# Optimization experiments

Measured on AMD Instinct MI355X. Metric: run time of the kernel, lower is better.

## Reference

```python
import jax, jax.numpy as jnp
import numpy as np
import math

B, S, D = 2, 2048, 512
N_BUCKETS = 64
N_HYP = int(math.log2(N_BUCKETS))  # 6


def setup_inputs() -> dict:
    key = jax.random.key(0)
    ks = jax.random.split(key, 6)
    x = jax.random.normal(ks[0], (B, S, D), dtype=jnp.float32)
    # torch.nn.Linear params: weight [out,in], bias [out]
    Wq = jax.random.normal(ks[1], (D, D), dtype=jnp.float32) / jnp.sqrt(D)
    bq = jax.random.normal(ks[2], (D,), dtype=jnp.float32) * 0.01
    Wv = jax.random.normal(ks[3], (D, D), dtype=jnp.float32) / jnp.sqrt(D)
    bv = jax.random.normal(ks[4], (D,), dtype=jnp.float32) * 0.01
    hyperplanes = jax.random.normal(ks[5], (D + 1, N_HYP), dtype=jnp.float32)
    return {"x": x, "Wq": Wq, "bq": bq, "Wv": Wv, "bv": bv, "hyperplanes": hyperplanes}


def _get_buckets(q, hyperplanes):
    # append constant-1 feature: [B,S,D+1]
    qa = jnp.concatenate([q, jnp.ones(q.shape[:2] + (1,), q.dtype)], axis=2)
    proj = jnp.einsum('bse,en->bsn', qa, hyperplanes)
    bits = (proj >= 0).astype(jnp.float32)
    powers = (2.0 ** jnp.arange(N_HYP)).astype(jnp.float32)
    return jnp.einsum('bsn,n->bs', bits, powers)  # [B,S] float bucket ids


def reference(x, Wq, bq, Wv, bv, hyperplanes):
    q = x @ Wq.T + bq
    v = x @ Wv.T + bv
    buckets = _get_buckets(q, hyperplanes)  # [B,S]
    scale = 1.0 / math.sqrt(D)

    def body(acc, i):
        # NOTE: faithful to source: tokens IN bucket i are zeroed (masked_fill
        # with mask = buckets == i), then full dense softmax attention.
        mask = (buckets == i)[..., None]  # [B,S,1]
        qb = jnp.where(mask, 0.0, q)
        vb = jnp.where(mask, 0.0, v)
        att = jax.nn.softmax(jnp.einsum('bsd,btd->bst', qb, qb) * scale, axis=-1)
        return acc + jnp.einsum('bst,btd->bsd', att, vb), None

    init = jnp.zeros_like(x)
    out, _ = jax.lax.scan(body, init, jnp.arange(N_BUCKETS, dtype=jnp.float32))
    return out
```

## Files before the change

kernel.cpp:

```cpp
#include <hip/hip_runtime.h>
#include <math.h>

#define B_ 2
#define S_ 2048
#define D_ 512
#define NB_ 64
#define NH_ 6
#define ROWS (B_*S_)
#define SCALE 0.044194173824159216f

typedef float f32x4 __attribute__((ext_vector_type(4)));
typedef __bf16 bf16v8 __attribute__((ext_vector_type(8)));
typedef short s16x8 __attribute__((ext_vector_type(8)));
typedef unsigned short u16x4 __attribute__((ext_vector_type(4)));

__device__ __forceinline__ float b2f(unsigned short u) {
    unsigned int v = (unsigned int)u << 16;
    float f; __builtin_memcpy(&f, &v, 4); return f;
}
__device__ __forceinline__ unsigned short f2b(float f) {
    unsigned int v; __builtin_memcpy(&v, &f, 4);
    v += 0x7fffu + ((v >> 16) & 1u);
    return (unsigned short)(v >> 16);
}

#define GLOAD16(g, l) __builtin_amdgcn_global_load_lds( \
    (const __attribute__((address_space(1))) unsigned int*)(g), \
    (__attribute__((address_space(3))) unsigned int*)(uintptr_t)(l), 16, 0, 0)

template<int EPI>
__global__ __launch_bounds__(256) void mfma_nt(
    const unsigned short* __restrict__ A, const unsigned short* __restrict__ B,
    int N, int K, long long zA, long long zB,
    float* __restrict__ Cf, long long zC,
    unsigned short* __restrict__ Ch, long long zCh,
    const float* __restrict__ e0, long long z0,
    const float* __restrict__ e1, long long z1,
    const int* __restrict__ ib, long long zi,
    const int* __restrict__ prm)
{
    __shared__ unsigned short Als[128 * 64];
    __shared__ unsigned short Bls[64 * 64];
    int tid = threadIdx.x;
    int w = tid >> 6, l = tid & 63;
    int wr = w >> 1, wc = w & 1;
    int zb = blockIdx.z;
    A += zb * zA;  B += zb * zB;
    if (prm) prm += (size_t)zb * S_;

    int gx = gridDim.x;
    int nwg = gx * gridDim.y;
    int lin = blockIdx.y * gx + blockIdx.x;
    int qq = nwg >> 3;
    int wg = (lin & 7) * qq + (lin >> 3);
    int m0 = (wg / gx) * 128, n0 = (wg % gx) * 64;

    const unsigned short* asrc[4];
    #pragma unroll
    for (int j = 0; j < 4; ++j) {
        int chunk = w * 4 + j;
        int r = chunk * 8 + (l >> 3);
        asrc[j] = A + (size_t)(m0 + r) * K + ((l & 7) ^ (l >> 3)) * 8;
    }
    const unsigned short* bsrc[2];
    #pragma unroll
    for (int j = 0; j < 2; ++j) {
        int chunk = w * 2 + j;
        int r = n0 + chunk * 8 + (l >> 3);
        if (prm) r = prm[r];
        bsrc[j] = B + (size_t)r * K + ((l & 7) ^ (l >> 3)) * 8;
    }

    f32x4 acc[4][2] = {};
    int rl = l & 15, hi = l >> 4;

    for (int k0 = 0; k0 < K; k0 += 64) {
        #pragma unroll
        for (int j = 0; j < 4; ++j) GLOAD16(asrc[j] + k0, Als + (w * 4 + j) * 512);
        #pragma unroll
        for (int j = 0; j < 2; ++j) GLOAD16(bsrc[j] + k0, Bls + (w * 2 + j) * 512);
        __syncthreads();
        bf16v8 af[4][2], bfr[2][2];
        const char* Ab = (const char*)Als;
        const char* Bb = (const char*)Bls;
        #pragma unroll
        for (int kk = 0; kk < 2; ++kk) {
            int kb = kk * 64 + hi * 16;
            #pragma unroll
            for (int f = 0; f < 4; ++f) {
                int ra = wr * 64 + f * 16 + rl;
                af[f][kk] = *(const bf16v8*)(Ab + ra * 128 + (kb ^ ((ra & 7) << 4)));
            }
            #pragma unroll
            for (int f = 0; f < 2; ++f) {
                int rb = wc * 32 + f * 16 + rl;
                bfr[f][kk] = *(const bf16v8*)(Bb + rb * 128 + (kb ^ ((rb & 7) << 4)));
            }
        }
        #pragma unroll
        for (int fm = 0; fm < 4; ++fm)
            #pragma unroll
            for (int fn = 0; fn < 2; ++fn)
                #pragma unroll
                for (int kk = 0; kk < 2; ++kk)
                    acc[fm][fn] = __builtin_amdgcn_mfma_f32_16x16x32_bf16(
                        af[fm][kk], bfr[fn][kk], acc[fm][fn], 0, 0, 0);
        __syncthreads();
    }

    if (EPI == 0) {
        int colBase = n0 + wc * 32;
        if (colBase < D_) {
            #pragma unroll
            for (int fm = 0; fm < 4; ++fm) {
                float p[4] = {0.f, 0.f, 0.f, 0.f};
                #pragma unroll
                for (int fn = 0; fn < 2; ++fn) {
                    int col = colBase + fn * 16 + rl;
                    float bs = e0[col];
                    #pragma unroll
                    for (int r = 0; r < 4; ++r) {
                        int row = m0 + wr * 64 + fm * 16 + hi * 4 + r;
                        float cv = acc[fm][fn][r] + bs;
                        unsigned short h = f2b(cv);
                        Ch[(size_t)row * D_ + col] = h;
                        float qb = b2f(h);
                        p[r] = fmaf(qb, qb, p[r]);
                    }
                }
                #pragma unroll
                for (int mask = 1; mask < 16; mask <<= 1)
                    #pragma unroll
                    for (int r = 0; r < 4; ++r) p[r] += __shfl_xor(p[r], mask);
                if (rl == 0) {
                    #pragma unroll
                    for (int r = 0; r < 4; ++r) {
                        int row = m0 + wr * 64 + fm * 16 + hi * 4 + r;
                        atomicAdd(&Cf[row], p[r]);
                    }
                }
            }
        } else {
            #pragma unroll
            for (int fm = 0; fm < 4; ++fm)
                #pragma unroll
                for (int fn = 0; fn < 2; ++fn) {
                    int col = colBase + fn * 16 + rl - D_;
                    float bs = e1[col];
                    #pragma unroll
                    for (int r = 0; r < 4; ++r) {
                        int row = m0 + wr * 64 + fm * 16 + hi * 4 + r;
                        ((float*)ib)[(size_t)row * D_ + col] = acc[fm][fn][r] + bs;
                    }
                }
        }
    } else {
        Ch += zb * zCh;  e0 += zb * z0;
        #pragma unroll
        for (int fm = 0; fm < 4; ++fm)
            #pragma unroll
            for (int fn = 0; fn < 2; ++fn) {
                int col = n0 + wc * 32 + fn * 16 + rl;
                #pragma unroll
                for (int r = 0; r < 4; ++r) {
                    int row = m0 + wr * 64 + fm * 16 + hi * 4 + r;
                    float ev = __expf(fmaf(acc[fm][fn][r], SCALE, -e0[row]));
                    Ch[(size_t)row * N + col] = f2b(ev);
                }
            }
    }
}

__global__ __launch_bounds__(256) void mfma_pv64(
    const unsigned short* __restrict__ Eh, const unsigned short* __restrict__ vT,
    const float* __restrict__ sumVall, const float* __restrict__ sumVb,
    const int* __restrict__ bucket, float* __restrict__ out)
{
    __shared__ unsigned short Als[64 * 64];
    __shared__ unsigned short Bls[64 * 64];
    int tid = threadIdx.x, w = tid >> 6, l = tid & 63;
    int wr = w >> 1, wc = w & 1, rl = l & 15, hi = l >> 4;
    int zb = blockIdx.z;
    const unsigned short* A  = Eh + (size_t)zb * S_ * S_;
    const unsigned short* Bv = vT + (size_t)zb * D_ * S_;
    const float* sva = sumVall + (size_t)zb * D_;
    const float* svb = sumVb + (size_t)zb * NB_ * D_;
    const int* bkt = bucket + (size_t)zb * S_;
    float* outb = out + (size_t)zb * S_ * D_;

    int lin = blockIdx.y * 8 + blockIdx.x;
    int xcd = lin & 7, rest = lin >> 3;
    int m0 = (((rest >> 3) << 3) | xcd) * 64;
    int n0 = (rest & 7) * 64;

    const unsigned short* asrc[2];
    const unsigned short* bsrc[2];
    #pragma unroll
    for (int j = 0; j < 2; ++j) {
        int chunk = w * 2 + j;
        int r = chunk * 8 + (l >> 3);
        int c = ((l & 7) ^ (l >> 3)) * 8;
        asrc[j] = A  + (size_t)(m0 + r) * S_ + c;
        bsrc[j] = Bv + (size_t)(n0 + r) * S_ + c;
    }

    f32x4 acc[2][2] = {};
    for (int k0 = 0; k0 < S_; k0 += 64) {
        #pragma unroll
        for (int j = 0; j < 2; ++j) GLOAD16(asrc[j] + k0, Als + (w * 2 + j) * 512);
        #pragma unroll
        for (int j = 0; j < 2; ++j) GLOAD16(bsrc[j] + k0, Bls + (w * 2 + j) * 512);
        __syncthreads();
        bf16v8 af[2][2], bfr[2][2];
        const char* Ab = (const char*)Als;
        const char* Bb = (const char*)Bls;
        #pragma unroll
        for (int kk = 0; kk < 2; ++kk) {
            int kb = kk * 64 + hi * 16;
            #pragma unroll
            for (int f = 0; f < 2; ++f) {
                int ra = wr * 32 + f * 16 + rl;
                af[f][kk] = *(const bf16v8*)(Ab + ra * 128 + (kb ^ ((ra & 7) << 4)));
                int rb = wc * 32 + f * 16 + rl;
                bfr[f][kk] = *(const bf16v8*)(Bb + rb * 128 + (kb ^ ((rb & 7) << 4)));
            }
        }
        #pragma unroll
        for (int fm = 0; fm < 2; ++fm)
            #pragma unroll
            for (int fn = 0; fn < 2; ++fn)
                #pragma unroll
                for (int kk = 0; kk < 2; ++kk)
                    acc[fm][fn] = __builtin_amdgcn_mfma_f32_16x16x32_bf16(
                        af[fm][kk], bfr[fn][kk], acc[fm][fn], 0, 0, 0);
        __syncthreads();
    }
    const float invS = 1.0f / (float)S_;
    #pragma unroll
    for (int fm = 0; fm < 2; ++fm)
        #pragma unroll
        for (int fn = 0; fn < 2; ++fn) {
            int col = n0 + wc * 32 + fn * 16 + rl;
            float sa = sva[col];
            #pragma unroll
            for (int r = 0; r < 4; ++r) {
                int row = m0 + wr * 32 + fm * 16 + hi * 4 + r;
                int bm = bkt[row];
                outb[(size_t)row * D_ + col] =
                    acc[fm][fn][r] + (sa - svb[(size_t)bm * D_ + col]) * invS;
            }
        }
}

__global__ void init_kernel(float* __restrict__ Mrow, int* __restrict__ cnt)
{
    int i = blockIdx.x * 256 + threadIdx.x;
    if (i < ROWS) Mrow[i] = 0.f;
    if (i < B_ * NB_) cnt[i] = 0;
}

__global__ void convert_bf16(const float* __restrict__ src, unsigned short* __restrict__ dst, int n)
{
    for (int i = (blockIdx.x * 256 + threadIdx.x) * 4; i < n; i += gridDim.x * 1024) {
        float4 f = *(const float4*)(src + i);
        u16x4 u = { f2b(f.x), f2b(f.y), f2b(f.z), f2b(f.w) };
        *(u16x4*)(dst + i) = u;
    }
}

__global__ __launch_bounds__(256) void transpose_v(
    const float* __restrict__ v, const int* __restrict__ perm,
    unsigned short* __restrict__ vT)
{
    __shared__ float tl[32][33];
    int b = blockIdx.z;
    int d0 = blockIdx.x * 32, s0 = blockIdx.y * 32;
    int tx = threadIdx.x & 31, ty = threadIdx.x >> 5;
    const float* vb = v + (size_t)b * S_ * D_;
    const int* pm = perm + (size_t)b * S_;
    #pragma unroll
    for (int i = 0; i < 4; ++i)
        tl[ty + i * 8][tx] = vb[(size_t)pm[s0 + ty + i * 8] * D_ + d0 + tx];
    __syncthreads();
    unsigned short* vt = vT + (size_t)b * D_ * S_;
    #pragma unroll
    for (int i = 0; i < 4; ++i)
        vt[(size_t)(d0 + ty + i * 8) * S_ + s0 + tx] = f2b(tl[tx][ty + i * 8]);
}

__global__ __launch_bounds__(64) void bucket_kernel(
    const unsigned short* __restrict__ qh, const float* __restrict__ H,
    int* __restrict__ bucket, float* __restrict__ Mrow)
{
    int row = blockIdx.x;
    int lane = threadIdx.x;
    const unsigned short* qr = qh + (size_t)row * D_;
    float proj[NH_] = {};
    for (int d = lane; d < D_; d += 64) {
        float qv = b2f(qr[d]);
        #pragma unroll
        for (int n = 0; n < NH_; ++n)
            proj[n] = fmaf(qv, H[d * NH_ + n], proj[n]);
    }
    #pragma unroll
    for (int off = 32; off; off >>= 1) {
        #pragma unroll
        for (int n = 0; n < NH_; ++n) proj[n] += __shfl_down(proj[n], off);
    }
    if (lane == 0) {
        int bk = 0;
        #pragma unroll
        for (int n = 0; n < NH_; ++n) {
            float p = proj[n] + H[D_ * NH_ + n];
            if (p >= 0.f) bk |= (1 << n);
        }
        bucket[row] = bk;
        Mrow[row] = Mrow[row] * SCALE;
    }
}

__global__ __launch_bounds__(256) void hist_kernel(
    const int* __restrict__ bucket, int* __restrict__ cnt, int* __restrict__ idxl)
{
    int r = blockIdx.x * 256 + threadIdx.x;
    int b = r / S_;
    int s = r - b * S_;
    int j = bucket[r];
    int pos = atomicAdd(&cnt[b * NB_ + j], 1);
    idxl[((size_t)(b * NB_ + j)) * S_ + pos] = s;
}

__global__ __launch_bounds__(64) void prefix_kernel(
    const int* __restrict__ cnt, int* __restrict__ off)
{
    int b = blockIdx.x;
    int j = threadIdx.x;
    int c = cnt[b * NB_ + j];
    int x = c;
    #pragma unroll
    for (int o = 1; o < 64; o <<= 1) {
        int y = __shfl_up(x, o);
        if (j >= o) x += y;
    }
    off[b * (NB_ + 1) + j] = x - c;
    if (j == 63) off[b * (NB_ + 1) + 64] = x;
}

__global__ __launch_bounds__(64) void permbuild_kernel(
    const int* __restrict__ idxl, const int* __restrict__ cnt,
    const int* __restrict__ off, int* __restrict__ perm, int* __restrict__ p2b)
{
    int j = blockIdx.x, b = blockIdx.y;
    int n = cnt[b * NB_ + j];
    int o = off[b * (NB_ + 1) + j];
    const int* lst = idxl + ((size_t)(b * NB_ + j)) * S_;
    for (int k = threadIdx.x; k < n; k += 64) {
        perm[(size_t)b * S_ + o + k] = lst[k];
        p2b[(size_t)b * S_ + o + k] = j;
    }
}

__global__ __launch_bounds__(256) void zwgamma_kernel(
    unsigned short* __restrict__ Eh, const int* __restrict__ p2b,
    const int* __restrict__ off, const int* __restrict__ cnt,
    const int* __restrict__ bucket, const float* __restrict__ Mrow)
{
    int row = blockIdx.x;
    int b = row >> 11;
    __shared__ float er[S_];
    __shared__ float zl[NB_];
    __shared__ float wl[NB_ + 1];
    int tid = threadIdx.x;
    unsigned short* Er = Eh + (size_t)row * S_;
    int t0 = tid * 8;
    s16x8 ev = *(const s16x8*)(Er + t0);
    #pragma unroll
    for (int i = 0; i < 8; ++i)
        er[t0 + i] = b2f((unsigned short)ev[i]);
    __syncthreads();
    {
        int j = tid >> 2, sub = tid & 3;
        int lo = off[b * (NB_ + 1) + j], hiX = off[b * (NB_ + 1) + j + 1];
        float z = 0.f;
        for (int k = lo + sub; k < hiX; k += 4) z += er[k];
        z += __shfl_xor(z, 1);
        z += __shfl_xor(z, 2);
        if (sub == 0) zl[j] = z;
    }
    __syncthreads();
    if (tid < NB_) {
        int j = tid;
        float zj = zl[j];
        float ztot = zj;
        #pragma unroll
        for (int o = 32; o; o >>= 1) ztot += __shfl_xor(ztot, o);
        int bs = bucket[row];
        float em = __expf(-Mrow[row]);
        float wj = 0.f;
        if (j != bs) wj = 1.0f / (ztot - zj + (float)cnt[b * NB_ + j] * em);
        float Wt = wj;
        #pragma unroll
        for (int o = 32; o; o >>= 1) Wt += __shfl_xor(Wt, o);
        wl[j] = wj;
        if (j == 0) wl[NB_] = Wt;
    }
    __syncthreads();
    float Wt = wl[NB_];
    const int* pb = p2b + (size_t)b * S_ + t0;
    int4 b0 = *(const int4*)pb;
    int4 b1 = *(const int4*)(pb + 4);
    s16x8 ov;
    ov[0] = (short)f2b(er[t0 + 0] * (Wt - wl[b0.x]));
    ov[1] = (short)f2b(er[t0 + 1] * (Wt - wl[b0.y]));
    ov[2] = (short)f2b(er[t0 + 2] * (Wt - wl[b0.z]));
    ov[3] = (short)f2b(er[t0 + 3] * (Wt - wl[b0.w]));
    ov[4] = (short)f2b(er[t0 + 4] * (Wt - wl[b1.x]));
    ov[5] = (short)f2b(er[t0 + 5] * (Wt - wl[b1.y]));
    ov[6] = (short)f2b(er[t0 + 6] * (Wt - wl[b1.z]));
    ov[7] = (short)f2b(er[t0 + 7] * (Wt - wl[b1.w]));
    *(s16x8*)(Er + t0) = ov;
}

__global__ __launch_bounds__(256) void sumv2_kernel(
    const float* __restrict__ v, const int* __restrict__ cnt,
    const int* __restrict__ idxl, float* __restrict__ sumVb)
{
    int j = blockIdx.x, b = blockIdx.y;
    int d = blockIdx.z * 256 + threadIdx.x;
    int n = cnt[b * NB_ + j];
    const int* lst = idxl + ((size_t)(b * NB_ + j)) * S_;
    const float* vb = v + (size_t)b * S_ * D_;
    float acc = 0.f;
    for (int k = 0; k < n; ++k)
        acc += vb[(size_t)lst[k] * D_ + d];
    sumVb[((size_t)b * NB_ + j) * D_ + d] = acc;
}

__global__ __launch_bounds__(256) void sumvall_kernel(
    const float* __restrict__ sumVb, float* __restrict__ sumVall)
{
    int b = blockIdx.y;
    int d = blockIdx.x * 256 + threadIdx.x;
    float acc = 0.f;
    for (int j = 0; j < NB_; ++j)
        acc += sumVb[((size_t)b * NB_ + j) * D_ + d];
    sumVall[b * D_ + d] = acc;
}

extern "C" void kernel_launch(void* const* d_in, const int* in_sizes, int n_in,
                              void* d_out, int out_size, void* d_ws, size_t ws_size,
                              hipStream_t stream) {
    (void)in_sizes; (void)n_in; (void)out_size; (void)ws_size;
    const float* x  = (const float*)d_in[0];
    const float* Wq = (const float*)d_in[1];
    const float* bq = (const float*)d_in[2];
    const float* Wv = (const float*)d_in[3];
    const float* bv = (const float*)d_in[4];
    const float* H  = (const float*)d_in[5];
    float* out = (float*)d_out;

    char* p = (char*)d_ws;
    auto alloc = [&](size_t bytes) -> char* {
        char* r = p; p += (bytes + 255) & ~(size_t)255; return r;
    };
    float* v       = (float*)alloc((size_t)ROWS * D_ * 4);
    float* Mrow    = (float*)alloc((size_t)ROWS * 4);
    float* sumVb   = (float*)alloc((size_t)B_ * NB_ * D_ * 4);
    float* sumVall = (float*)alloc((size_t)B_ * D_ * 4);
    int*   bucket  = (int*)alloc((size_t)ROWS * 4);
    int*   cnt     = (int*)alloc((size_t)B_ * NB_ * 4);
    int*   offb    = (int*)alloc((size_t)B_ * (NB_ + 1) * 4);
    int*   perm    = (int*)alloc((size_t)B_ * S_ * 4);
    int*   p2b     = (int*)alloc((size_t)B_ * S_ * 4);
    int*   idxl    = (int*)alloc((size_t)B_ * NB_ * S_ * 4);
    unsigned short* xh   = (unsigned short*)alloc((size_t)ROWS * D_ * 2);
    unsigned short* qh   = (unsigned short*)alloc((size_t)ROWS * D_ * 2);
    unsigned short* Wqvh = (unsigned short*)alloc((size_t)2 * D_ * D_ * 2);
    unsigned short* vTh  = (unsigned short*)alloc((size_t)B_ * D_ * S_ * 2);
    unsigned short* Eh   = (unsigned short*)alloc((size_t)B_ * S_ * S_ * 2);

    init_kernel<<<ROWS / 256, 256, 0, stream>>>(Mrow, cnt);
    convert_bf16<<<2048, 256, 0, stream>>>(x, xh, ROWS * D_);
    convert_bf16<<<256, 256, 0, stream>>>(Wq, Wqvh, D_ * D_);
    convert_bf16<<<256, 256, 0, stream>>>(Wv, Wqvh + (size_t)D_ * D_, D_ * D_);
    mfma_nt<0><<<dim3(2 * D_ / 64, ROWS / 128, 1), 256, 0, stream>>>(
        xh, Wqvh, 2 * D_, D_, 0, 0, Mrow, 0, qh, 0, bq, 0, bv, 0, (int*)v, 0, nullptr);
    bucket_kernel<<<ROWS, 64, 0, stream>>>(qh, H, bucket, Mrow);
    hist_kernel<<<ROWS / 256, 256, 0, stream>>>(bucket, cnt, idxl);
    prefix_kernel<<<B_, 64, 0, stream>>>(cnt, offb);
    permbuild_kernel<<<dim3(NB_, B_), 64, 0, stream>>>(idxl, cnt, offb, perm, p2b);
    sumv2_kernel<<<dim3(NB_, B_, D_ / 256), 256, 0, stream>>>(v, cnt, idxl, sumVb);
    sumvall_kernel<<<dim3(D_ / 256, B_), 256, 0, stream>>>(sumVb, sumVall);
    transpose_v<<<dim3(D_ / 32, S_ / 32, B_), 256, 0, stream>>>(v, perm, vTh);
    mfma_nt<1><<<dim3(S_ / 64, S_ / 128, B_), 256, 0, stream>>>(
        qh, qh, S_, D_, (long long)S_ * D_, (long long)S_ * D_,
        nullptr, 0, Eh, (long long)S_ * S_, Mrow, S_, nullptr, 0, nullptr, 0, perm);
    zwgamma_kernel<<<ROWS, 256, 0, stream>>>(Eh, p2b, offb, cnt, bucket, Mrow);
    mfma_pv64<<<dim3(D_ / 64, S_ / 64, B_), 256, 0, stream>>>(
        Eh, vTh, sumVall, sumVb, bucket, out);
}
```

Measured before the change: 116.2 us.

## Merge small prep kernels and widen QK^T tile to 128x128

Folds init and the three bf16 conversions into one prep kernel. Merges the histogram into the bucket kernel and prefix with perm build, and replaces the sumVall reduction with atomics inside sumv2. Splits the templated GEMM into a projection kernel and a dedicated QK kernel whose tile grows from 128x64 to 128x128 for more reuse. This cuts launch count and global traffic, at the cost of a serial per-bucket perm loop, more registers, and fewer workgroups for the QK GEMM.

```diff
diff --git a/kernel.cpp b/kernel.cpp
--- a/kernel.cpp
+++ b/kernel.cpp
@@ -28,25 +28,44 @@
     (const __attribute__((address_space(1))) unsigned int*)(g), \
     (__attribute__((address_space(3))) unsigned int*)(uintptr_t)(l), 16, 0, 0)
 
-template<int EPI>
-__global__ __launch_bounds__(256) void mfma_nt(
+__global__ void prep_kernel(
+    const float* __restrict__ x, unsigned short* __restrict__ xh,
+    const float* __restrict__ Wq, const float* __restrict__ Wv,
+    unsigned short* __restrict__ Wqvh,
+    float* __restrict__ Mrow, int* __restrict__ cnt, float* __restrict__ sumVall)
+{
+    int t = blockIdx.x * 256 + threadIdx.x;
+    int stride = gridDim.x * 256;
+    for (int i = t; i < ROWS * D_ / 4; i += stride) {
+        float4 f = ((const float4*)x)[i];
+        u16x4 u = { f2b(f.x), f2b(f.y), f2b(f.z), f2b(f.w) };
+        ((u16x4*)xh)[i] = u;
+    }
+    for (int i = t; i < D_ * D_ / 4; i += stride) {
+        float4 f = ((const float4*)Wq)[i];
+        u16x4 u = { f2b(f.x), f2b(f.y), f2b(f.z), f2b(f.w) };
+        ((u16x4*)Wqvh)[i] = u;
+        float4 g = ((const float4*)Wv)[i];
+        u16x4 w = { f2b(g.x), f2b(g.y), f2b(g.z), f2b(g.w) };
+        ((u16x4*)(Wqvh + (size_t)D_ * D_))[i] = w;
+    }
+    for (int i = t; i < ROWS; i += stride) Mrow[i] = 0.f;
+    for (int i = t; i < B_ * NB_; i += stride) cnt[i] = 0;
+    for (int i = t; i < B_ * D_; i += stride) sumVall[i] = 0.f;
+}
+
+__global__ __launch_bounds__(256) void mfma_proj(
     const unsigned short* __restrict__ A, const unsigned short* __restrict__ B,
-    int N, int K, long long zA, long long zB,
-    float* __restrict__ Cf, long long zC,
-    unsigned short* __restrict__ Ch, long long zCh,
-    const float* __restrict__ e0, long long z0,
-    const float* __restrict__ e1, long long z1,
-    const int* __restrict__ ib, long long zi,
-    const int* __restrict__ prm)
+    const float* __restrict__ bq, const float* __restrict__ bv,
+    float* __restrict__ MrowRaw, unsigned short* __restrict__ qh,
+    float* __restrict__ v)
 {
     __shared__ unsigned short Als[128 * 64];
     __shared__ unsigned short Bls[64 * 64];
+    const int K = D_, N = 2 * D_;
     int tid = threadIdx.x;
     int w = tid >> 6, l = tid & 63;
     int wr = w >> 1, wc = w & 1;
-    int zb = blockIdx.z;
-    A += zb * zA;  B += zb * zB;
-    if (prm) prm += (size_t)zb * S_;
 
     int gx = gridDim.x;
     int nwg = gx * gridDim.y;
@@ -67,7 +86,6 @@
     for (int j = 0; j < 2; ++j) {
         int chunk = w * 2 + j;
         int r = n0 + chunk * 8 + (l >> 3);
-        if (prm) r = prm[r];
         bsrc[j] = B + (size_t)r * K + ((l & 7) ^ (l >> 3)) * 8;
     }
 
@@ -108,66 +126,134 @@
         __syncthreads();
     }
 
-    if (EPI == 0) {
-        int colBase = n0 + wc * 32;
-        if (colBase < D_) {
-            #pragma unroll
-            for (int fm = 0; fm < 4; ++fm) {
-                float p[4] = {0.f, 0.f, 0.f, 0.f};
-                #pragma unroll
-                for (int fn = 0; fn < 2; ++fn) {
-                    int col = colBase + fn * 16 + rl;
-                    float bs = e0[col];
-                    #pragma unroll
-                    for (int r = 0; r < 4; ++r) {
-                        int row = m0 + wr * 64 + fm * 16 + hi * 4 + r;
-                        float cv = acc[fm][fn][r] + bs;
-                        unsigned short h = f2b(cv);
-                        Ch[(size_t)row * D_ + col] = h;
-                        float qb = b2f(h);
-                        p[r] = fmaf(qb, qb, p[r]);
-                    }
-                }
-                #pragma unroll
-                for (int mask = 1; mask < 16; mask <<= 1)
-                    #pragma unroll
-                    for (int r = 0; r < 4; ++r) p[r] += __shfl_xor(p[r], mask);
-                if (rl == 0) {
-                    #pragma unroll
-                    for (int r = 0; r < 4; ++r) {
-                        int row = m0 + wr * 64 + fm * 16 + hi * 4 + r;
-                        atomicAdd(&Cf[row], p[r]);
-                    }
-                }
-            }
-        } else {
-            #pragma unroll
-            for (int fm = 0; fm < 4; ++fm)
-                #pragma unroll
-                for (int fn = 0; fn < 2; ++fn) {
-                    int col = colBase + fn * 16 + rl - D_;
-                    float bs = e1[col];
-                    #pragma unroll
-                    for (int r = 0; r < 4; ++r) {
-                        int row = m0 + wr * 64 + fm * 16 + hi * 4 + r;
-                        ((float*)ib)[(size_t)row * D_ + col] = acc[fm][fn][r] + bs;
-                    }
-                }
-        }
-    } else {
-        Ch += zb * zCh;  e0 += zb * z0;
-        #pragma unroll
-        for (int fm = 0; fm < 4; ++fm)
+    int colBase = n0 + wc * 32;
+    if (colBase < D_) {
+        #pragma unroll
+        for (int fm = 0; fm < 4; ++fm) {
+            float p[4] = {0.f, 0.f, 0.f, 0.f};
             #pragma unroll
             for (int fn = 0; fn < 2; ++fn) {
-                int col = n0 + wc * 32 + fn * 16 + rl;
+                int col = colBase + fn * 16 + rl;
+                float bs = bq[col];
                 #pragma unroll
                 for (int r = 0; r < 4; ++r) {
                     int row = m0 + wr * 64 + fm * 16 + hi * 4 + r;
-                    float ev = __expf(fmaf(acc[fm][fn][r], SCALE, -e0[row]));
-                    Ch[(size_t)row * N + col] = f2b(ev);
+                    float cv = acc[fm][fn][r] + bs;
+                    unsigned short h = f2b(cv);
+                    qh[(size_t)row * D_ + col] = h;
+                    float qb = b2f(h);
+                    p[r] = fmaf(qb, qb, p[r]);
                 }
             }
+            #pragma unroll
+            for (int mask = 1; mask < 16; mask <<= 1)
+                #pragma unroll
+                for (int r = 0; r < 4; ++r) p[r] += __shfl_xor(p[r], mask);
+            if (rl == 0) {
+                #pragma unroll
+                for (int r = 0; r < 4; ++r) {
+                    int row = m0 + wr * 64 + fm * 16 + hi * 4 + r;
+                    atomicAdd(&MrowRaw[row], p[r]);
+                }
+            }
+        }
+    } else {
+        #pragma unroll
+        for (int fm = 0; fm < 4; ++fm)
+            #pragma unroll
+            for (int fn = 0; fn < 2; ++fn) {
+                int col = colBase + fn * 16 + rl - D_;
+                float bs = bv[col];
+                #pragma unroll
+                for (int r = 0; r < 4; ++r) {
+                    int row = m0 + wr * 64 + fm * 16 + hi * 4 + r;
+                    v[(size_t)row * D_ + col] = acc[fm][fn][r] + bs;
+                }
+            }
+    }
+}
+
+__global__ __launch_bounds__(256) void mfma_qk(
+    const unsigned short* __restrict__ qh, const int* __restrict__ prm,
+    const float* __restrict__ Mrow, unsigned short* __restrict__ Eh)
+{
+    __shared__ unsigned short Als[128 * 64];
+    __shared__ unsigned short Bls[128 * 64];
+    const int K = D_;
+    int tid = threadIdx.x;
+    int w = tid >> 6, l = tid & 63;
+    int wr = w >> 1, wc = w & 1;
+    int zb = blockIdx.z;
+    const unsigned short* A = qh + (size_t)zb * S_ * D_;
+    prm += (size_t)zb * S_;
+    const float* Mb = Mrow + (size_t)zb * S_;
+    unsigned short* Eb = Eh + (size_t)zb * S_ * S_;
+
+    int gx = gridDim.x;
+    int nwg = gx * gridDim.y;
+    int lin = blockIdx.y * gx + blockIdx.x;
+    int qq = nwg >> 3;
+    int wg = (lin & 7) * qq + (lin >> 3);
+    int m0 = (wg / gx) * 128, n0 = (wg % gx) * 128;
+
+    const unsigned short* asrc[4];
+    const unsigned short* bsrc[4];
+    #pragma unroll
+    for (int j = 0; j < 4; ++j) {
+        int chunk = w * 4 + j;
+        int r = chunk * 8 + (l >> 3);
+        int c = ((l & 7) ^ (l >> 3)) * 8;
+        asrc[j] = A + (size_t)(m0 + r) * K + c;
+        bsrc[j] = A + (size_t)prm[n0 + r] * K + c;
+    }
+
+    f32x4 acc[4][4] = {};
+    int rl = l & 15, hi = l >> 4;
+
+    for (int k0 = 0; k0 < K; k0 += 64) {
+        #pragma unroll
+        for (int j = 0; j < 4; ++j) GLOAD16(asrc[j] + k0, Als + (w * 4 + j) * 512);
+        #pragma unroll
+        for (int j = 0; j < 4; ++j) GLOAD16(bsrc[j] + k0, Bls + (w * 4 + j) * 512);
+        __syncthreads();
+        bf16v8 af[4][2], bfr[4][2];
+        const char* Ab = (const char*)Als;
+        const char* Bb = (const char*)Bls;
+        #pragma unroll
+        for (int kk = 0; kk < 2; ++kk) {
+            int kb = kk * 64 + hi * 16;
+            #pragma unroll
+            for (int f = 0; f < 4; ++f) {
+                int ra = wr * 64 + f * 16 + rl;
+                af[f][kk] = *(const bf16v8*)(Ab + ra * 128 + (kb ^ ((ra & 7) << 4)));
+                int rb = wc * 64 + f * 16 + rl;
+                bfr[f][kk] = *(const bf16v8*)(Bb + rb * 128 + (kb ^ ((rb & 7) << 4)));
+            }
+        }
+        #pragma unroll
+        for (int fm = 0; fm < 4; ++fm)
+            #pragma unroll
+            for (int fn = 0; fn < 4; ++fn)
+                #pragma unroll
+                for (int kk = 0; kk < 2; ++kk)
+                    acc[fm][fn] = __builtin_amdgcn_mfma_f32_16x16x32_bf16(
+                        af[fm][kk], bfr[fn][kk], acc[fm][fn], 0, 0, 0);
+        __syncthreads();
+    }
+
+    #pragma unroll
+    for (int fm = 0; fm < 4; ++fm) {
+        #pragma unroll
+        for (int r = 0; r < 4; ++r) {
+            int row = m0 + wr * 64 + fm * 16 + hi * 4 + r;
+            float m = Mb[row];
+            #pragma unroll
+            for (int fn = 0; fn < 4; ++fn) {
+                int col = n0 + wc * 64 + fn * 16 + rl;
+                float ev = __expf(fmaf(acc[fm][fn][r], SCALE, -m));
+                Eb[(size_t)row * S_ + col] = f2b(ev);
+            }
+        }
     }
 }
 
@@ -252,22 +338,6 @@
         }
 }
 
-__global__ void init_kernel(float* __restrict__ Mrow, int* __restrict__ cnt)
-{
-    int i = blockIdx.x * 256 + threadIdx.x;
-    if (i < ROWS) Mrow[i] = 0.f;
-    if (i < B_ * NB_) cnt[i] = 0;
-}
-
-__global__ void convert_bf16(const float* __restrict__ src, unsigned short* __restrict__ dst, int n)
-{
-    for (int i = (blockIdx.x * 256 + threadIdx.x) * 4; i < n; i += gridDim.x * 1024) {
-        float4 f = *(const float4*)(src + i);
-        u16x4 u = { f2b(f.x), f2b(f.y), f2b(f.z), f2b(f.w) };
-        *(u16x4*)(dst + i) = u;
-    }
-}
-
 __global__ __launch_bounds__(256) void transpose_v(
     const float* __restrict__ v, const int* __restrict__ perm,
     unsigned short* __restrict__ vT)
@@ -290,14 +360,18 @@
 
 __global__ __launch_bounds__(64) void bucket_kernel(
     const unsigned short* __restrict__ qh, const float* __restrict__ H,
-    int* __restrict__ bucket, float* __restrict__ Mrow)
+    int* __restrict__ bucket, float* __restrict__ Mrow,
+    int* __restrict__ cnt, int* __restrict__ idxl)
 {
     int row = blockIdx.x;
     int lane = threadIdx.x;
     const unsigned short* qr = qh + (size_t)row * D_;
     float proj[NH_] = {};
-    for (int d = lane; d < D_; d += 64) {
-        float qv = b2f(qr[d]);
+    s16x8 qv8 = *(const s16x8*)(qr + lane * 8);
+    #pragma unroll
+    for (int i = 0; i < 8; ++i) {
+        float qv = b2f((unsigned short)qv8[i]);
+        int d = lane * 8 + i;
         #pragma unroll
         for (int n = 0; n < NH_; ++n)
             proj[n] = fmaf(qv, H[d * NH_ + n], proj[n]);
@@ -316,22 +390,15 @@
         }
         bucket[row] = bk;
         Mrow[row] = Mrow[row] * SCALE;
-    }
-}
-
-__global__ __launch_bounds__(256) void hist_kernel(
-    const int* __restrict__ bucket, int* __restrict__ cnt, int* __restrict__ idxl)
-{
-    int r = blockIdx.x * 256 + threadIdx.x;
-    int b = r / S_;
-    int s = r - b * S_;
-    int j = bucket[r];
-    int pos = atomicAdd(&cnt[b * NB_ + j], 1);
-    idxl[((size_t)(b * NB_ + j)) * S_ + pos] = s;
-}
-
-__global__ __launch_bounds__(64) void prefix_kernel(
-    const int* __restrict__ cnt, int* __restrict__ off)
+        int b = row >> 11, s = row & (S_ - 1);
+        int pos = atomicAdd(&cnt[b * NB_ + bk], 1);
+        idxl[((size_t)(b * NB_ + bk)) * S_ + pos] = s;
+    }
+}
+
+__global__ __launch_bounds__(64) void permprefix_kernel(
+    const int* __restrict__ cnt, const int* __restrict__ idxl,
+    int* __restrict__ off, int* __restrict__ perm, int* __restrict__ p2b)
 {
     int b = blockIdx.x;
     int j = threadIdx.x;
@@ -342,19 +409,11 @@
         int y = __shfl_up(x, o);
         if (j >= o) x += y;
     }
-    off[b * (NB_ + 1) + j] = x - c;
+    int o = x - c;
+    off[b * (NB_ + 1) + j] = o;
     if (j == 63) off[b * (NB_ + 1) + 64] = x;
-}
-
-__global__ __launch_bounds__(64) void permbuild_kernel(
-    const int* __restrict__ idxl, const int* __restrict__ cnt,
-    const int* __restrict__ off, int* __restrict__ perm, int* __restrict__ p2b)
-{
-    int j = blockIdx.x, b = blockIdx.y;
-    int n = cnt[b * NB_ + j];
-    int o = off[b * (NB_ + 1) + j];
     const int* lst = idxl + ((size_t)(b * NB_ + j)) * S_;
-    for (int k = threadIdx.x; k < n; k += 64) {
+    for (int k = 0; k < c; ++k) {
         perm[(size_t)b * S_ + o + k] = lst[k];
         p2b[(size_t)b * S_ + o + k] = j;
     }
@@ -423,7 +482,8 @@
 
 __global__ __launch_bounds__(256) void sumv2_kernel(
     const float* __restrict__ v, const int* __restrict__ cnt,
-    const int* __restrict__ idxl, float* __restrict__ sumVb)
+    const int* __restrict__ idxl, float* __restrict__ sumVb,
+    float* __restrict__ sumVall)
 {
     int j = blockIdx.x, b = blockIdx.y;
     int d = blockIdx.z * 256 + threadIdx.x;
@@ -434,17 +494,7 @@
     for (int k = 0; k < n; ++k)
         acc += vb[(size_t)lst[k] * D_ + d];
     sumVb[((size_t)b * NB_ + j) * D_ + d] = acc;
-}
-
-__global__ __launch_bounds__(256) void sumvall_kernel(
-    const float* __restrict__ sumVb, float* __restrict__ sumVall)
-{
-    int b = blockIdx.y;
-    int d = blockIdx.x * 256 + threadIdx.x;
-    float acc = 0.f;
-    for (int j = 0; j < NB_; ++j)
-        acc += sumVb[((size_t)b * NB_ + j) * D_ + d];
-    sumVall[b * D_ + d] = acc;
+    atomicAdd(&sumVall[b * D_ + d], acc);
 }
 
 extern "C" void kernel_launch(void* const* d_in, const int* in_sizes, int n_in,
@@ -479,22 +529,14 @@
     unsigned short* vTh  = (unsigned short*)alloc((size_t)B_ * D_ * S_ * 2);
     unsigned short* Eh   = (unsigned short*)alloc((size_t)B_ * S_ * S_ * 2);
 
-    init_kernel<<<ROWS / 256, 256, 0, stream>>>(Mrow, cnt);
-    convert_bf16<<<2048, 256, 0, stream>>>(x, xh, ROWS * D_);
-    convert_bf16<<<256, 256, 0, stream>>>(Wq, Wqvh, D_ * D_);
-    convert_bf16<<<256, 256, 0, stream>>>(Wv, Wqvh + (size_t)D_ * D_, D_ * D_);
-    mfma_nt<0><<<dim3(2 * D_ / 64, ROWS / 128, 1), 256, 0, stream>>>(
-        xh, Wqvh, 2 * D_, D_, 0, 0, Mrow, 0, qh, 0, bq, 0, bv, 0, (int*)v, 0, nullptr);
-    bucket_kernel<<<ROWS, 64, 0, stream>>>(qh, H, bucket, Mrow);
-    hist_kernel<<<ROWS / 256, 256, 0, stream>>>(bucket, cnt, idxl);
-    prefix_kernel<<<B_, 64, 0, stream>>>(cnt, offb);
-    permbuild_kernel<<<dim3(NB_, B_), 64, 0, stream>>>(idxl, cnt, offb, perm, p2b);
-    sumv2_kernel<<<dim3(NB_, B_, D_ / 256), 256, 0, stream>>>(v, cnt, idxl, sumVb);
-    sumvall_kernel<<<dim3(D_ / 256, B_), 256, 0, stream>>>(sumVb, sumVall);
+    prep_kernel<<<2048, 256, 0, stream>>>(x, xh, Wq, Wv, Wqvh, Mrow, cnt, sumVall);
+    mfma_proj<<<dim3(2 * D_ / 64, ROWS / 128, 1), 256, 0, stream>>>(
+        xh, Wqvh, bq, bv, Mrow, qh, v);
+    bucket_kernel<<<ROWS, 64, 0, stream>>>(qh, H, bucket, Mrow, cnt, idxl);
+    permprefix_kernel<<<B_, 64, 0, stream>>>(cnt, idxl, offb, perm, p2b);
+    sumv2_kernel<<<dim3(NB_, B_, D_ / 256), 256, 0, stream>>>(v, cnt, idxl, sumVb, sumVall);
     transpose_v<<<dim3(D_ / 32, S_ / 32, B_), 256, 0, stream>>>(v, perm, vTh);
-    mfma_nt<1><<<dim3(S_ / 64, S_ / 128, B_), 256, 0, stream>>>(
-        qh, qh, S_, D_, (long long)S_ * D_, (long long)S_ * D_,
-        nullptr, 0, Eh, (long long)S_ * S_, Mrow, S_, nullptr, 0, nullptr, 0, perm);
+    mfma_qk<<<dim3(S_ / 128, S_ / 128, B_), 256, 0, stream>>>(qh, perm, Mrow, Eh);
     zwgamma_kernel<<<ROWS, 256, 0, stream>>>(Eh, p2b, offb, cnt, bucket, Mrow);
     mfma_pv64<<<dim3(D_ / 64, S_ / 64, B_), 256, 0, stream>>>(
         Eh, vTh, sumVall, sumVb, bucket, out);
```

Result: faster. 111.3 us (-4.2%).
